# Performance work log

Measured on AMD Instinct MI355X. Metric: run time of the kernel, lower is better.

Reference implementation:

```python
import jax, jax.numpy as jnp
import numpy as np

N = 2048
MAX_ITER = 1000          # hardcoded in XGR.forward (max_iter=1000)
TOL = 1e-6               # symmetric_sinkhorn default tol
WEIGHT_LOSS_XGR = 250.0  # init kwarg weight_loss_XGR


def setup_inputs() -> dict:
    key = jax.random.key(0)
    k1, k2 = jax.random.split(key)
    A = jax.random.normal(k1, (N, N), dtype=jnp.float32)
    M = jnp.abs(A + A.T)  # symmetric, non-negative cost matrix
    group = jax.random.uniform(k2, (N, N), dtype=jnp.float32,
                               minval=1e-3, maxval=1.0)  # positive (log taken)
    return {"M": M, "group": group, "eps": 1}


def reference(M, group, eps):
    eps = jnp.asarray(eps, M.dtype)
    n = M.shape[0]

    def converged(f):
        # rows of log_T = (f_i + f_j - C_ij)/eps must sum (in prob domain) to 1
        log_T = (f[:, None] + f[None, :] - M) / eps
        row_sums = jnp.exp(jax.nn.logsumexp(log_T, axis=-1))
        return jnp.all(jnp.abs(row_sums - 1.0) < TOL)

    def cond_fn(state):
        _, k, done = state
        return jnp.logical_and(k < MAX_ITER, jnp.logical_not(done))

    def body_fn(state):
        f, k, _ = state
        # torch: f = 0.5*(f - eps*logsumexp((f - C)/eps, -1)); f broadcasts over rows
        f = 0.5 * (f - eps * jax.nn.logsumexp((f[None, :] - M) / eps, axis=-1))
        done = jax.lax.cond(k % 10 == 0, converged,
                            lambda _: jnp.array(False), f)
        return (f, k + 1, done)

    f0 = jnp.zeros((n,), dtype=M.dtype)
    f, _, _ = jax.lax.while_loop(cond_fn, body_fn,
                                 (f0, jnp.int32(0), jnp.array(False)))

    log_Q = (f[:, None] + f[None, :] - M) / eps
    loss = (group * (jnp.log(group) - log_Q - 1.0) + jnp.exp(log_Q)).sum()
    return WEIGHT_LOSS_XGR * loss
```

## Files before the change

### kernel.cpp

```cpp
#include <hip/hip_runtime.h>
#include <hip/hip_cooperative_groups.h>
#include <math.h>

namespace cg = cooperative_groups;

#define NN 2048
#define MAX_ITER 1000
#define TOLF 1e-6f
#define TPB 512
#define NBLK 256
#define WPB 8
#define SPIN_LIMIT (1 << 14)

__device__ __forceinline__ unsigned long long pack_pair(unsigned int tag,
                                                        unsigned int viol,
                                                        float v) {
    return ((unsigned long long)((tag << 1) | viol) << 32) | (unsigned long long)__float_as_uint(v);
}

__global__ __launch_bounds__(TPB, 1)
void xgr_sinkhorn(const float* __restrict__ Mm,
                  const float* __restrict__ Gg,
                  const int* __restrict__ eps_p,
                  float* __restrict__ out,
                  unsigned long long* __restrict__ ws64)
{
    __shared__ float  m_lds[WPB][NN];
    __shared__ float  fA[NN], fB[NN];
    __shared__ int    s_stale[WPB];
    __shared__ int    s_viol[WPB];
    __shared__ int    s_abort;
    __shared__ double s_part[WPB];

    unsigned long long* gb0 = ws64;
    unsigned long long* gb1 = ws64 + NN;
    double* acc      = (double*)(ws64 + 2 * NN);
    int*    done_cnt = (int*)(ws64 + 2 * NN + 1);
    int*    abortp   = (int*)(ws64 + 2 * NN + 2);

    const int tid  = threadIdx.x;
    const int lane = tid & 63;
    const int wave = tid >> 6;
    const int row  = blockIdx.x * WPB + wave;
    const int gtid = blockIdx.x * TPB + tid;

    if (tid < WPB) {
        const int r = blockIdx.x * WPB + tid;
        gb0[r] = 0ULL;
        gb1[r] = 0xFFFFFFFF00000000ULL;
    }
    if (gtid == 0) { *acc = 0.0; *done_cnt = 0; *abortp = 0; }
    if (tid == 0)  s_abort = 0;

    const int ebits = *eps_p;
    const float eps = (ebits >= 1 && ebits <= (1 << 20)) ? (float)ebits
                                                         : __int_as_float(ebits);
    const float inv_eps = 1.0f / eps;

    {
        const float4* Mrow = (const float4*)(Mm + (size_t)row * NN);
        float4* ml4 = (float4*)m_lds[wave];
        #pragma unroll
        for (int k = 0; k < 8; ++k) {
            const int idx = (k << 6) + lane;
            ml4[idx] = Mrow[idx];
        }
    }

    cg::this_grid().sync();

    float* f_final = nullptr;
    bool   aborted = false;

    for (int t = 0; ; ++t) {
        float* fl = (t & 1) ? fB : fA;
        unsigned long long* gb  = (t & 1) ? gb1 : gb0;
        unsigned long long* gbn = (t & 1) ? gb0 : gb1;

        {
            bool ok0 = false, ok1 = false, ok2 = false, ok3 = false;
            int violloc = 0;
            const unsigned int want = (unsigned int)t;
            int guard = 0;
            for (;;) {
                if (!ok0) {
                    unsigned long long p = __hip_atomic_load(&gb[tid], __ATOMIC_RELAXED, __HIP_MEMORY_SCOPE_AGENT);
                    if ((unsigned int)(p >> 33) == want) {
                        ok0 = true; violloc |= (int)((p >> 32) & 1ULL);
                        fl[tid] = __uint_as_float((unsigned int)p);
                    }
                }
                if (!ok1) {
                    unsigned long long p = __hip_atomic_load(&gb[tid + 512], __ATOMIC_RELAXED, __HIP_MEMORY_SCOPE_AGENT);
                    if ((unsigned int)(p >> 33) == want) {
                        ok1 = true; violloc |= (int)((p >> 32) & 1ULL);
                        fl[tid + 512] = __uint_as_float((unsigned int)p);
                    }
                }
                if (!ok2) {
                    unsigned long long p = __hip_atomic_load(&gb[tid + 1024], __ATOMIC_RELAXED, __HIP_MEMORY_SCOPE_AGENT);
                    if ((unsigned int)(p >> 33) == want) {
                        ok2 = true; violloc |= (int)((p >> 32) & 1ULL);
                        fl[tid + 1024] = __uint_as_float((unsigned int)p);
                    }
                }
                if (!ok3) {
                    unsigned long long p = __hip_atomic_load(&gb[tid + 1536], __ATOMIC_RELAXED, __HIP_MEMORY_SCOPE_AGENT);
                    if ((unsigned int)(p >> 33) == want) {
                        ok3 = true; violloc |= (int)((p >> 32) & 1ULL);
                        fl[tid + 1536] = __uint_as_float((unsigned int)p);
                    }
                }
                const int anybad = __any(!(ok0 && ok1 && ok2 && ok3)) ? 1 : 0;
                if (lane == 0) s_stale[wave] = anybad;
                if (tid == 0 && (guard & 63) == 63)
                    if (__hip_atomic_load(abortp, __ATOMIC_RELAXED, __HIP_MEMORY_SCOPE_AGENT))
                        s_abort = 1;
                __syncthreads();
                const int blk = s_stale[0] | s_stale[1] | s_stale[2] | s_stale[3]
                              | s_stale[4] | s_stale[5] | s_stale[6] | s_stale[7];
                const int ab  = s_abort;
                __syncthreads();
                if (!blk) break;
                if (ab || ++guard > SPIN_LIMIT) {
                    if (tid == 0)
                        __hip_atomic_store(abortp, 1, __ATOMIC_RELAXED, __HIP_MEMORY_SCOPE_AGENT);
                    aborted = true;
                    break;
                }
            }
            if (aborted) { f_final = fl; break; }

            if ((t % 10) == 2) {
                const int wv = __any(violloc != 0) ? 1 : 0;
                if (lane == 0) s_viol[wave] = wv;
                __syncthreads();
                const int bv = s_viol[0] | s_viol[1] | s_viol[2] | s_viol[3]
                             | s_viol[4] | s_viol[5] | s_viol[6] | s_viol[7];
                if (bv == 0) {
                    f_final = (t & 1) ? fA : fB;
                    break;
                }
            }
        }
        if (t == MAX_ITER) {
            f_final = fl;
            break;
        }

        const float4* ml4 = (const float4*)m_lds[wave];
        const float4* fl4 = (const float4*)fl;
        float x[32];
        float mloc = -INFINITY;
        #pragma unroll
        for (int k = 0; k < 8; ++k) {
            const int idx = (k << 6) + lane;
            const float4 mv = ml4[idx];
            const float4 f4 = fl4[idx];
            const float x0 = (f4.x - mv.x) * inv_eps;
            const float x1 = (f4.y - mv.y) * inv_eps;
            const float x2 = (f4.z - mv.z) * inv_eps;
            const float x3 = (f4.w - mv.w) * inv_eps;
            x[4*k+0] = x0; x[4*k+1] = x1; x[4*k+2] = x2; x[4*k+3] = x3;
            mloc = fmaxf(mloc, fmaxf(fmaxf(x0, x1), fmaxf(x2, x3)));
        }
        float mw = mloc;
        #pragma unroll
        for (int off = 32; off; off >>= 1)
            mw = fmaxf(mw, __shfl_down(mw, off));
        mw = __shfl(mw, 0);
        float s = 0.0f;
        #pragma unroll
        for (int k = 0; k < 32; ++k) s += expf(x[k] - mw);
        #pragma unroll
        for (int off = 32; off; off >>= 1)
            s += __shfl_down(s, off);

        if (lane == 0) {
            const float L  = mw + logf(s);
            const float fi = fl[row];
            const float fn = 0.5f * (fi - eps * L);
            unsigned int viol = 0u;
            if ((t % 10) == 1) {
                const float rs = expf(fi * inv_eps + L);
                viol = (fabsf(rs - 1.0f) < TOLF) ? 0u : 1u;
            }
            __hip_atomic_store(&gbn[row], pack_pair((unsigned int)(t + 1), viol, fn),
                               __ATOMIC_RELAXED, __HIP_MEMORY_SCOPE_AGENT);
        }
    }

    __syncthreads();
    const float4* Grow = (const float4*)(Gg + (size_t)row * NN);
    const float4* ml4  = (const float4*)m_lds[wave];
    const float4* fl4  = (const float4*)f_final;
    const float   fi   = f_final[row];
    double lsum = 0.0;
    #pragma unroll
    for (int k = 0; k < 8; ++k) {
        const int idx = (k << 6) + lane;
        const float4 mv = ml4[idx];
        const float4 gv = Grow[idx];
        const float4 f4 = fl4[idx];
        {
            const float lq = (fi + f4.x - mv.x) * inv_eps;
            lsum += (double)(gv.x * (logf(gv.x) - lq - 1.0f) + expf(lq));
        }
        {
            const float lq = (fi + f4.y - mv.y) * inv_eps;
            lsum += (double)(gv.y * (logf(gv.y) - lq - 1.0f) + expf(lq));
        }
        {
            const float lq = (fi + f4.z - mv.z) * inv_eps;
            lsum += (double)(gv.z * (logf(gv.z) - lq - 1.0f) + expf(lq));
        }
        {
            const float lq = (fi + f4.w - mv.w) * inv_eps;
            lsum += (double)(gv.w * (logf(gv.w) - lq - 1.0f) + expf(lq));
        }
    }
    #pragma unroll
    for (int off = 32; off; off >>= 1)
        lsum += __shfl_down(lsum, off);

    if (lane == 0) s_part[wave] = lsum;
    __syncthreads();
    if (tid == 0) {
        double b = 0.0;
        #pragma unroll
        for (int w = 0; w < WPB; ++w) b += s_part[w];
        atomicAdd(acc, b);
        __threadfence();
        const int prev = __hip_atomic_fetch_add(done_cnt, 1,
                                                __ATOMIC_RELAXED, __HIP_MEMORY_SCOPE_AGENT);
        if (prev == NBLK - 1) {
            __threadfence();
            const double total = __hip_atomic_load(acc, __ATOMIC_RELAXED,
                                                   __HIP_MEMORY_SCOPE_AGENT);
            out[0] = (float)(250.0 * total);
        }
    }
}

extern "C" void kernel_launch(void* const* d_in, const int* in_sizes, int n_in,
                              void* d_out, int out_size, void* d_ws, size_t ws_size,
                              hipStream_t stream)
{
    const float* Mm    = (const float*)d_in[0];
    const float* Gg    = (const float*)d_in[1];
    const int*   eps_p = (const int*)d_in[2];
    float* out = (float*)d_out;
    unsigned long long* ws64 = (unsigned long long*)d_ws;

    void* args[] = { (void*)&Mm, (void*)&Gg, (void*)&eps_p, (void*)&out, (void*)&ws64 };
    hipLaunchCooperativeKernel((void*)xgr_sinkhorn, dim3(NBLK), dim3(TPB),
                               args, 0, stream);
}
```

Baseline: 240.2 us.

## Replace block-wide barriers in f gather with per-wave LDS flags

Each wave now polls a contiguous 256-entry slice of the global f buffer, writes it to LDS, and publishes a per-wave LDS flag carrying the iteration tag and a violation bit. The other waves in the block wait on these flags chunk by chunk instead of meeting at two __syncthreads per spin iteration. This is meant to cut block-level barrier overhead and let compute on ready chunks start before the whole vector has arrived. In exchange it adds LDS spin-waits with s_sleep and relies on fence ordering between the LDS data and flag writes, which could introduce ordering bugs or hangs if the flag protocol is wrong.

New measurement: 298.5 us. +24.3%, slower.

```diff
diff --git a/kernel.cpp b/kernel.cpp
--- a/kernel.cpp
+++ b/kernel.cpp
@@ -11,6 +11,8 @@
 #define NBLK 256
 #define WPB 8
 #define SPIN_LIMIT (1 << 14)
+#define LDS_SPIN_LIMIT (1 << 18)
+#define FLAG_ABORT 0x7f000000
 
 __device__ __forceinline__ unsigned long long pack_pair(unsigned int tag,
                                                         unsigned int viol,
@@ -27,16 +29,14 @@
 {
     __shared__ float  m_lds[WPB][NN];
     __shared__ float  fA[NN], fB[NN];
-    __shared__ int    s_stale[WPB];
-    __shared__ int    s_viol[WPB];
-    __shared__ int    s_abort;
+    __shared__ int    sflag[2][WPB];
     __shared__ double s_part[WPB];
 
     unsigned long long* gb0 = ws64;
     unsigned long long* gb1 = ws64 + NN;
-    double* acc      = (double*)(ws64 + 2 * NN);
-    int*    done_cnt = (int*)(ws64 + 2 * NN + 1);
-    int*    abortp   = (int*)(ws64 + 2 * NN + 2);
+    double*       acc      = (double*)(ws64 + 2 * NN);
+    unsigned int* done_cnt = (unsigned int*)(ws64 + 2 * NN + 1);
+    unsigned int* abortp   = done_cnt + 1;
 
     const int tid  = threadIdx.x;
     const int lane = tid & 63;
@@ -49,8 +49,8 @@
         gb0[r] = 0ULL;
         gb1[r] = 0xFFFFFFFF00000000ULL;
     }
-    if (gtid == 0) { *acc = 0.0; *done_cnt = 0; *abortp = 0; }
-    if (tid == 0)  s_abort = 0;
+    if (gtid == 0) { *acc = 0.0; *done_cnt = 0u; *abortp = 0u; }
+    if (tid < 2 * WPB) ((int*)sflag)[tid] = -1;
 
     const int ebits = *eps_p;
     const float eps = (ebits >= 1 && ebits <= (1 << 20)) ? (float)ebits
@@ -73,97 +73,90 @@
     bool   aborted = false;
 
     for (int t = 0; ; ++t) {
-        float* fl = (t & 1) ? fB : fA;
-        unsigned long long* gb  = (t & 1) ? gb1 : gb0;
-        unsigned long long* gbn = (t & 1) ? gb0 : gb1;
-
-        {
+        const int p = t & 1;
+        float* fl = p ? fB : fA;
+        unsigned long long* gb  = p ? gb1 : gb0;
+        unsigned long long* gbn = p ? gb0 : gb1;
+
+        {
+            const unsigned int want = (unsigned int)t;
+            unsigned long long* gw = gb + (wave << 8) + (lane << 2);
+            unsigned long long pw0 = 0, pw1 = 0, pw2 = 0, pw3 = 0;
             bool ok0 = false, ok1 = false, ok2 = false, ok3 = false;
-            int violloc = 0;
-            const unsigned int want = (unsigned int)t;
-            int guard = 0;
+            int vio = 0, guard = 0;
             for (;;) {
-                if (!ok0) {
-                    unsigned long long p = __hip_atomic_load(&gb[tid], __ATOMIC_RELAXED, __HIP_MEMORY_SCOPE_AGENT);
-                    if ((unsigned int)(p >> 33) == want) {
-                        ok0 = true; violloc |= (int)((p >> 32) & 1ULL);
-                        fl[tid] = __uint_as_float((unsigned int)p);
+                if (!ok0) { unsigned long long q = __hip_atomic_load(gw + 0, __ATOMIC_RELAXED, __HIP_MEMORY_SCOPE_AGENT);
+                            if ((unsigned int)(q >> 33) == want) { ok0 = true; pw0 = q; vio |= (int)((q >> 32) & 1ULL); } }
+                if (!ok1) { unsigned long long q = __hip_atomic_load(gw + 1, __ATOMIC_RELAXED, __HIP_MEMORY_SCOPE_AGENT);
+                            if ((unsigned int)(q >> 33) == want) { ok1 = true; pw1 = q; vio |= (int)((q >> 32) & 1ULL); } }
+                if (!ok2) { unsigned long long q = __hip_atomic_load(gw + 2, __ATOMIC_RELAXED, __HIP_MEMORY_SCOPE_AGENT);
+                            if ((unsigned int)(q >> 33) == want) { ok2 = true; pw2 = q; vio |= (int)((q >> 32) & 1ULL); } }
+                if (!ok3) { unsigned long long q = __hip_atomic_load(gw + 3, __ATOMIC_RELAXED, __HIP_MEMORY_SCOPE_AGENT);
+                            if ((unsigned int)(q >> 33) == want) { ok3 = true; pw3 = q; vio |= (int)((q >> 32) & 1ULL); } }
+                if (__all(ok0 && ok1 && ok2 && ok3)) break;
+                if ((++guard & 63) == 0) {
+                    int ab = 0;
+                    if (lane == 0) ab = (int)__hip_atomic_load(abortp, __ATOMIC_RELAXED, __HIP_MEMORY_SCOPE_AGENT);
+                    ab = __shfl(ab, 0);
+                    if (ab || guard > SPIN_LIMIT) {
+                        if (lane == 0) __hip_atomic_store(abortp, 1u, __ATOMIC_RELAXED, __HIP_MEMORY_SCOPE_AGENT);
+                        aborted = true; break;
                     }
                 }
-                if (!ok1) {
-                    unsigned long long p = __hip_atomic_load(&gb[tid + 512], __ATOMIC_RELAXED, __HIP_MEMORY_SCOPE_AGENT);
-                    if ((unsigned int)(p >> 33) == want) {
-                        ok1 = true; violloc |= (int)((p >> 32) & 1ULL);
-                        fl[tid + 512] = __uint_as_float((unsigned int)p);
-                    }
-                }
-                if (!ok2) {
-                    unsigned long long p = __hip_atomic_load(&gb[tid + 1024], __ATOMIC_RELAXED, __HIP_MEMORY_SCOPE_AGENT);
-                    if ((unsigned int)(p >> 33) == want) {
-                        ok2 = true; violloc |= (int)((p >> 32) & 1ULL);
-                        fl[tid + 1024] = __uint_as_float((unsigned int)p);
-                    }
-                }
-                if (!ok3) {
-                    unsigned long long p = __hip_atomic_load(&gb[tid + 1536], __ATOMIC_RELAXED, __HIP_MEMORY_SCOPE_AGENT);
-                    if ((unsigned int)(p >> 33) == want) {
-                        ok3 = true; violloc |= (int)((p >> 32) & 1ULL);
-                        fl[tid + 1536] = __uint_as_float((unsigned int)p);
-                    }
-                }
-                const int anybad = __any(!(ok0 && ok1 && ok2 && ok3)) ? 1 : 0;
-                if (lane == 0) s_stale[wave] = anybad;
-                if (tid == 0 && (guard & 63) == 63)
-                    if (__hip_atomic_load(abortp, __ATOMIC_RELAXED, __HIP_MEMORY_SCOPE_AGENT))
-                        s_abort = 1;
-                __syncthreads();
-                const int blk = s_stale[0] | s_stale[1] | s_stale[2] | s_stale[3]
-                              | s_stale[4] | s_stale[5] | s_stale[6] | s_stale[7];
-                const int ab  = s_abort;
-                __syncthreads();
-                if (!blk) break;
-                if (ab || ++guard > SPIN_LIMIT) {
-                    if (tid == 0)
-                        __hip_atomic_store(abortp, 1, __ATOMIC_RELAXED, __HIP_MEMORY_SCOPE_AGENT);
-                    aborted = true;
-                    break;
-                }
             }
-            if (aborted) { f_final = fl; break; }
-
-            if ((t % 10) == 2) {
-                const int wv = __any(violloc != 0) ? 1 : 0;
-                if (lane == 0) s_viol[wave] = wv;
-                __syncthreads();
-                const int bv = s_viol[0] | s_viol[1] | s_viol[2] | s_viol[3]
-                             | s_viol[4] | s_viol[5] | s_viol[6] | s_viol[7];
-                if (bv == 0) {
-                    f_final = (t & 1) ? fA : fB;
-                    break;
-                }
-            }
-        }
-        if (t == MAX_ITER) {
-            f_final = fl;
-            break;
-        }
-
-        const float4* ml4 = (const float4*)m_lds[wave];
-        const float4* fl4 = (const float4*)fl;
+            float4 v;
+            v.x = __uint_as_float((unsigned int)pw0);
+            v.y = __uint_as_float((unsigned int)pw1);
+            v.z = __uint_as_float((unsigned int)pw2);
+            v.w = __uint_as_float((unsigned int)pw3);
+            ((float4*)(fl + (wave << 8)))[lane] = v;
+            const int wv = __any(vio != 0) ? 1 : 0;
+            __threadfence_block();
+            if (lane == 0)
+                *(volatile int*)&sflag[p][wave] = aborted ? FLAG_ABORT : ((t << 1) | wv);
+        }
+        if (aborted) { f_final = fl; break; }
+
         float x[32];
         float mloc = -INFINITY;
-        #pragma unroll
-        for (int k = 0; k < 8; ++k) {
-            const int idx = (k << 6) + lane;
-            const float4 mv = ml4[idx];
-            const float4 f4 = fl4[idx];
+        int violall = 0;
+        const float4* ml4 = (const float4*)m_lds[wave];
+        for (int c = 0; c < WPB; ++c) {
+            volatile int* fp = &sflag[p][c];
+            int v = *fp;
+            int g = 0;
+            while (v < (t << 1)) {
+                __builtin_amdgcn_s_sleep(1);
+                if ((++g & 1023) == 0) {
+                    int ab = 0;
+                    if (lane == 0) ab = (int)__hip_atomic_load(abortp, __ATOMIC_RELAXED, __HIP_MEMORY_SCOPE_AGENT);
+                    ab = __shfl(ab, 0);
+                    if (ab || g > LDS_SPIN_LIMIT) { aborted = true; break; }
+                }
+                v = *fp;
+            }
+            if (aborted || v >= FLAG_ABORT) { aborted = true; break; }
+            violall |= (v & 1);
+            const float4 f4 = ((const float4*)(fl + (c << 8)))[lane];
+            const float4 mv = ml4[(c << 6) + lane];
             const float x0 = (f4.x - mv.x) * inv_eps;
             const float x1 = (f4.y - mv.y) * inv_eps;
             const float x2 = (f4.z - mv.z) * inv_eps;
             const float x3 = (f4.w - mv.w) * inv_eps;
-            x[4*k+0] = x0; x[4*k+1] = x1; x[4*k+2] = x2; x[4*k+3] = x3;
+            x[4*c+0] = x0; x[4*c+1] = x1; x[4*c+2] = x2; x[4*c+3] = x3;
             mloc = fmaxf(mloc, fmaxf(fmaxf(x0, x1), fmaxf(x2, x3)));
         }
+        if (aborted) {
+            if (lane == 0) __hip_atomic_store(abortp, 1u, __ATOMIC_RELAXED, __HIP_MEMORY_SCOPE_AGENT);
+            f_final = fl; break;
+        }
+
+        if ((t % 10) == 2 && violall == 0) {
+            f_final = p ? fA : fB;
+            break;
+        }
+        if (t == MAX_ITER) { f_final = fl; break; }
+
         float mw = mloc;
         #pragma unroll
         for (int off = 32; off; off >>= 1)
@@ -231,8 +224,8 @@
         for (int w = 0; w < WPB; ++w) b += s_part[w];
         atomicAdd(acc, b);
         __threadfence();
-        const int prev = __hip_atomic_fetch_add(done_cnt, 1,
-                                                __ATOMIC_RELAXED, __HIP_MEMORY_SCOPE_AGENT);
+        const unsigned int prev = __hip_atomic_fetch_add(done_cnt, 1u,
+                                                         __ATOMIC_RELAXED, __HIP_MEMORY_SCOPE_AGENT);
         if (prev == NBLK - 1) {
             __threadfence();
             const double total = __hip_atomic_load(acc, __ATOMIC_RELAXED,
```
